# Performance work log

Measured on AMD Instinct MI355X. Metric: run time of the kernel, lower is better.

Reference implementation:

```python
import jax, jax.numpy as jnp
import numpy as np
from jax import lax

STD_H, STD_W = 364, 280
RADIUS, SIGMA = 15, 4.0


def gaussian_kernel():
    r = jnp.arange(-RADIUS, RADIUS + 1, dtype=jnp.float32)
    d2 = r[:, None] ** 2 + r[None, :] ** 2
    k = jnp.exp(-0.5 / (SIGMA ** 2) * d2)
    k = k / k.sum()
    return k[None, None]  # (1,1,31,31) OIHW


def setup_inputs() -> dict:
    key = jax.random.key(0)
    k1, k2 = jax.random.split(key)
    B, H, W = 32, 512, 512
    input_face = jax.random.uniform(k1, (B, 3, H, W), dtype=jnp.float32)
    # landmarks in (x, y) pixel coords within the HxW image
    landmarks = jax.random.uniform(k2, (B, 68, 2), dtype=jnp.float32) * jnp.array([W, H], jnp.float32)
    weight = gaussian_kernel()
    return {"input_face": input_face, "landmarks": landmarks, "weight": weight}


def _blur(x, weight):
    # x: (B,1,h,w), 31x31 'same' conv (kernel symmetric, so corr == conv)
    return lax.conv_general_dilated(x, weight, (1, 1), 'SAME',
                                    dimension_numbers=('NCHW', 'OIHW', 'NCHW'))


def reference(input_face, landmarks, weight):
    B, C, H, W = input_face.shape
    scaling = STD_H / H
    lm = landmarks * scaling                      # (B,68,2) in standard coords
    center = lm[:, 30:31, :]                      # (B,1,2)

    p0 = lm[:, 30:36, :]
    p1 = lm[:, 2:15, :]
    p2 = lm[:, 48:68, :]
    p3 = lm[:, 6:11, :]
    p01 = (p0 - center) * 1.5 + center
    p11 = (p1 - center) * 0.5 + center
    p12 = (p1 - center) * 0.7 + center
    p13 = (p1 - center) * 0.9 + center
    p21 = (p2 - center) * 1.3 + center
    keys = jnp.concatenate([p0, p01, p12, p13, p11, p2, p3, p21], axis=-2)  # (B,96,2)

    iy = jnp.round(jnp.clip(keys[..., 1], 0, STD_H - 1)).astype(jnp.int32)
    ix = jnp.round(jnp.clip(keys[..., 0], 0, STD_W - 1)).astype(jnp.int32)

    # Faithful to torch advanced-indexing semantics: union of ALL batches'
    # points is written into every batch's heatmap.
    hm = jnp.zeros((STD_H, STD_W), jnp.float32).at[iy.ravel(), ix.ravel()].set(1.0)
    hm = jnp.broadcast_to(hm[None, None], (B, 1, STD_H, STD_W))

    w1 = _blur(hm, weight)
    w2 = jnp.where(w1 > 1e-7, 1.0, w1)
    w3 = _blur(w2, weight)

    w_mask = jax.image.resize(w3, (B, 1, H, W), method='bilinear')
    return (1.0 - w_mask) * input_face  # filling='black'
```

## Files before the change

### kernel.cpp

```cpp
#include <hip/hip_runtime.h>

#define BB   32
#define HH   512
#define WW   512
#define SH   364
#define SW   280
#define RAD  15
#define NK   96
#define OMN  (HH*WW)
#define PF4  (OMN/4)

#define OH   16
#define OW   32
#define NRM  13
#define NCM  19
#define WRM  (NRM + 2*RAD)
#define HRM  (NRM + 4*RAD)
#define HCP  84
#define WCP  52
#define NCP  20
#define G1   13
#define G2   5

typedef float f4 __attribute__((ext_vector_type(4)));

__device__ __forceinline__ void point_ij(const float* __restrict__ lm, int b, int j,
                                         int& ix, int& iy) {
    int idx; float s;
    if      (j <  6) { idx = 30 + j;        s = 1.0f; }
    else if (j < 12) { idx = 30 + (j - 6);  s = 1.5f; }
    else if (j < 25) { idx =  2 + (j - 12); s = 0.7f; }
    else if (j < 38) { idx =  2 + (j - 25); s = 0.9f; }
    else if (j < 51) { idx =  2 + (j - 38); s = 0.5f; }
    else if (j < 71) { idx = 48 + (j - 51); s = 1.0f; }
    else if (j < 76) { idx =  6 + (j - 71); s = 1.0f; }
    else             { idx = 48 + (j - 76); s = 1.3f; }
    const float scal = 364.0f / 512.0f;
    float lx = lm[b * 136 + idx * 2 + 0] * scal;
    float ly = lm[b * 136 + idx * 2 + 1] * scal;
    float kx, ky;
    if (s == 1.0f) { kx = lx; ky = ly; }
    else {
        float cx = lm[b * 136 + 30 * 2 + 0] * scal;
        float cy = lm[b * 136 + 30 * 2 + 1] * scal;
        kx = (lx - cx) * s + cx;
        ky = (ly - cy) * s + cy;
    }
    ix = __float2int_rn(fminf(fmaxf(kx, 0.0f), (float)(SW - 1)));
    iy = __float2int_rn(fminf(fmaxf(ky, 0.0f), (float)(SH - 1)));
}

__global__ __launch_bounds__(256, 2) void k_fused(const float* __restrict__ lm,
                                                  const float* __restrict__ wt,
                                                  const f4* __restrict__ face,
                                                  f4* __restrict__ out) {
    __shared__ float gwl[31];
    __shared__ alignas(16) float hmS[HRM][HCP];
    __shared__ alignas(16) float t1 [HRM][WCP];
    __shared__ alignas(16) float w2S[WRM][WCP];
    __shared__ alignas(16) float t2 [WRM][NCP];
    __shared__ alignas(16) float w3S[NRM][NCP];
    __shared__ alignas(16) float maskS[OH][OW];

    const int tid = threadIdx.x;
    const int h0 = blockIdx.y * OH, w0 = blockIdx.x * OW;
    const float sy = (float)SH / (float)HH;
    const float sx = (float)SW / (float)WW;

    const int j   = tid & 127;
    const int grp = tid >> 7;
    const int dh  = j >> 3, dw4 = (j & 7) << 2;
    const long off = (long)(h0 + dh) * (WW / 4) + ((w0 + dw4) >> 2);

    if (tid < 31) gwl[tid] = wt[15 * 31 + tid] / sqrtf(wt[15 * 31 + 15]);

    const int hl = h0 + OH - 1, wl = w0 + OW - 1;
    float fy0 = fmaxf(((float)h0 + 0.5f) * sy - 0.5f, 0.0f);
    float fyl = fminf(((float)hl + 0.5f) * sy - 0.5f, (float)(SH - 1));
    int rbase = (int)fy0;
    int rend  = min(SH - 1, (int)fyl + 1);
    float fx0 = fmaxf(((float)w0 + 0.5f) * sx - 0.5f, 0.0f);
    float fxl = fminf(((float)wl + 0.5f) * sx - 0.5f, (float)(SW - 1));
    int cbase = (int)fx0;
    int cend  = min(SW - 1, (int)fxl + 1);
    int NR = rend - rbase + 1;
    int NC = cend - cbase + 1;
    int HR = NR + 4 * RAD, HC = NC + 4 * RAD;

    for (int i = tid; i < HRM * HCP; i += 256) ((float*)hmS)[i] = 0.0f;
    __syncthreads();

    float g[31];
    #pragma unroll
    for (int k = 0; k < 31; ++k) g[k] = gwl[k];

    for (int p = tid; p < BB * NK; p += 256) {
        int b = p / NK, jj = p - b * NK;
        int ix, iy;
        point_ij(lm, b, jj, ix, iy);
        int ly = iy - (rbase - 2 * RAD), lx = ix - (cbase - 2 * RAD);
        if (ly >= 0 && ly < HR && lx >= 0 && lx < HC) hmS[ly][lx] = 1.0f;
    }

    f4 pf0  = face[(long)(grp +  0) * PF4 + off];
    f4 pf1  = face[(long)(grp +  2) * PF4 + off];
    f4 pf2  = face[(long)(grp +  4) * PF4 + off];
    f4 pf3  = face[(long)(grp +  6) * PF4 + off];
    f4 pf4  = face[(long)(grp +  8) * PF4 + off];
    f4 pf5  = face[(long)(grp + 10) * PF4 + off];
    f4 pf6  = face[(long)(grp + 12) * PF4 + off];
    f4 pf7  = face[(long)(grp + 14) * PF4 + off];
    f4 pf8  = face[(long)(grp + 16) * PF4 + off];
    f4 pf9  = face[(long)(grp + 18) * PF4 + off];
    f4 pf10 = face[(long)(grp + 20) * PF4 + off];
    f4 pf11 = face[(long)(grp + 22) * PF4 + off];
    f4 pf12 = face[(long)(grp + 24) * PF4 + off];
    f4 pf13 = face[(long)(grp + 26) * PF4 + off];
    f4 pf14 = face[(long)(grp + 28) * PF4 + off];
    f4 pf15 = face[(long)(grp + 30) * PF4 + off];

    __syncthreads();

    for (int it = tid; it < HRM * G1; it += 256) {
        int y = it / G1, c0g = it - y * G1;
        f4 rb[9];
        #pragma unroll
        for (int k = 0; k < 9; ++k) rb[k] = *(const f4*)&hmS[y][(c0g + k) * 4];
        float r[36];
        #pragma unroll
        for (int k = 0; k < 9; ++k) {
            r[4*k+0] = rb[k][0]; r[4*k+1] = rb[k][1];
            r[4*k+2] = rb[k][2]; r[4*k+3] = rb[k][3];
        }
        f4 o;
        #pragma unroll
        for (int q = 0; q < 4; ++q) {
            float acc = 0.0f;
            #pragma unroll
            for (int d = 0; d < 31; ++d) acc += g[d] * r[q + d];
            o[q] = acc;
        }
        *(f4*)&t1[y][c0g * 4] = o;
    }
    __syncthreads();

    for (int it = tid; it < WRM * G1; it += 256) {
        int y = it / G1, c0 = (it - y * G1) * 4;
        f4 acc = {0.0f, 0.0f, 0.0f, 0.0f};
        #pragma unroll
        for (int d = 0; d < 31; ++d) {
            f4 v = *(const f4*)&t1[y + d][c0];
            acc += v * g[d];
        }
        int gy = rbase - RAD + y;
        bool rowok = (gy >= 0 && gy < SH);
        f4 o;
        #pragma unroll
        for (int q = 0; q < 4; ++q) {
            float v = acc[q];
            v = (v > 1e-7f) ? 1.0f : v;
            int gx = cbase - RAD + c0 + q;
            o[q] = (rowok && gx >= 0 && gx < SW) ? v : 0.0f;
        }
        *(f4*)&w2S[y][c0] = o;
    }
    __syncthreads();

    for (int it = tid; it < WRM * G2; it += 256) {
        int y = it / G2, c0g = it - y * G2;
        f4 rb[9];
        #pragma unroll
        for (int k = 0; k < 9; ++k) rb[k] = *(const f4*)&w2S[y][(c0g + k) * 4];
        float r[36];
        #pragma unroll
        for (int k = 0; k < 9; ++k) {
            r[4*k+0] = rb[k][0]; r[4*k+1] = rb[k][1];
            r[4*k+2] = rb[k][2]; r[4*k+3] = rb[k][3];
        }
        f4 o;
        #pragma unroll
        for (int q = 0; q < 4; ++q) {
            float acc = 0.0f;
            #pragma unroll
            for (int d = 0; d < 31; ++d) acc += g[d] * r[q + d];
            o[q] = acc;
        }
        *(f4*)&t2[y][c0g * 4] = o;
    }
    __syncthreads();

    for (int it = tid; it < NRM * G2; it += 256) {
        int y = it / G2, c0 = (it - y * G2) * 4;
        f4 acc = {0.0f, 0.0f, 0.0f, 0.0f};
        #pragma unroll
        for (int d = 0; d < 31; ++d) {
            f4 v = *(const f4*)&t2[y + d][c0];
            acc += v * g[d];
        }
        *(f4*)&w3S[y][c0] = acc;
    }
    __syncthreads();

    for (int i = tid; i < OH * OW; i += 256) {
        int ddh = i / OW, ddw = i - ddh * OW;
        int h = h0 + ddh, w = w0 + ddw;
        float fy = fminf(fmaxf(((float)h + 0.5f) * sy - 0.5f, 0.0f), (float)(SH - 1));
        float fx = fminf(fmaxf(((float)w + 0.5f) * sx - 0.5f, 0.0f), (float)(SW - 1));
        int y0 = (int)fy, x0 = (int)fx;
        int y1 = min(y0 + 1, SH - 1), x1 = min(x0 + 1, SW - 1);
        float ty = fy - (float)y0, tx = fx - (float)x0;
        int ly0 = y0 - rbase, ly1 = y1 - rbase;
        int lx0 = x0 - cbase, lx1 = x1 - cbase;
        float v00 = w3S[ly0][lx0], v01 = w3S[ly0][lx1];
        float v10 = w3S[ly1][lx0], v11 = w3S[ly1][lx1];
        float v = (1.0f - ty) * ((1.0f - tx) * v00 + tx * v01)
                +         ty  * ((1.0f - tx) * v10 + tx * v11);
        maskS[ddh][ddw] = 1.0f - v;
    }
    __syncthreads();

    const f4 m = *(const f4*)&maskS[dh][dw4];
    __builtin_nontemporal_store(pf0  * m, &out[(long)(grp +  0) * PF4 + off]);
    __builtin_nontemporal_store(pf1  * m, &out[(long)(grp +  2) * PF4 + off]);
    __builtin_nontemporal_store(pf2  * m, &out[(long)(grp +  4) * PF4 + off]);
    __builtin_nontemporal_store(pf3  * m, &out[(long)(grp +  6) * PF4 + off]);
    __builtin_nontemporal_store(pf4  * m, &out[(long)(grp +  8) * PF4 + off]);
    __builtin_nontemporal_store(pf5  * m, &out[(long)(grp + 10) * PF4 + off]);
    __builtin_nontemporal_store(pf6  * m, &out[(long)(grp + 12) * PF4 + off]);
    __builtin_nontemporal_store(pf7  * m, &out[(long)(grp + 14) * PF4 + off]);
    __builtin_nontemporal_store(pf8  * m, &out[(long)(grp + 16) * PF4 + off]);
    __builtin_nontemporal_store(pf9  * m, &out[(long)(grp + 18) * PF4 + off]);
    __builtin_nontemporal_store(pf10 * m, &out[(long)(grp + 20) * PF4 + off]);
    __builtin_nontemporal_store(pf11 * m, &out[(long)(grp + 22) * PF4 + off]);
    __builtin_nontemporal_store(pf12 * m, &out[(long)(grp + 24) * PF4 + off]);
    __builtin_nontemporal_store(pf13 * m, &out[(long)(grp + 26) * PF4 + off]);
    __builtin_nontemporal_store(pf14 * m, &out[(long)(grp + 28) * PF4 + off]);
    __builtin_nontemporal_store(pf15 * m, &out[(long)(grp + 30) * PF4 + off]);
    #pragma unroll 8
    for (int k = 16; k < 48; ++k) {
        long idx = (long)(grp + 2 * k) * PF4 + off;
        f4 a = face[idx];
        __builtin_nontemporal_store(a * m, &out[idx]);
    }
}

extern "C" void kernel_launch(void* const* d_in, const int* in_sizes, int n_in,
                              void* d_out, int out_size, void* d_ws, size_t ws_size,
                              hipStream_t stream) {
    const float* face = (const float*)d_in[0];
    const float* lm   = (const float*)d_in[1];
    const float* wt   = (const float*)d_in[2];

    k_fused<<<dim3(WW / OW, HH / OH), 256, 0, stream>>>(
        lm, wt, (const f4*)face, (f4*)d_out);
}
```

Before: 50.98 us.

## Double output tile height and alias w2 buffer onto heatmap shared memory

Each block now covers a 32x32 output tile instead of 16x32, so the 31-tap blur halo is amortised over twice as many output pixels and the grid shrinks by half. Each thread now owns one float4 position and loops over all 96 batch-channel planes, instead of splitting planes between two thread groups. To keep shared memory within budget at the larger tile, the w2 buffer reuses the heatmap buffer's storage. The cost is fewer blocks for latency hiding and more serial memory work per thread, and the aliasing is only safe if the heatmap is fully consumed before w2 is written.

```diff
diff --git a/kernel.cpp b/kernel.cpp
--- a/kernel.cpp
+++ b/kernel.cpp
@@ -10,9 +10,9 @@
 #define OMN  (HH*WW)
 #define PF4  (OMN/4)
 
-#define OH   16
+#define OH   32
 #define OW   32
-#define NRM  13
+#define NRM  25
 #define NCM  19
 #define WRM  (NRM + 2*RAD)
 #define HRM  (NRM + 4*RAD)
@@ -57,19 +57,17 @@
     __shared__ float gwl[31];
     __shared__ alignas(16) float hmS[HRM][HCP];
     __shared__ alignas(16) float t1 [HRM][WCP];
-    __shared__ alignas(16) float w2S[WRM][WCP];
     __shared__ alignas(16) float t2 [WRM][NCP];
     __shared__ alignas(16) float w3S[NRM][NCP];
     __shared__ alignas(16) float maskS[OH][OW];
+    float (*w2S)[WCP] = (float(*)[WCP])hmS;
 
     const int tid = threadIdx.x;
     const int h0 = blockIdx.y * OH, w0 = blockIdx.x * OW;
     const float sy = (float)SH / (float)HH;
     const float sx = (float)SW / (float)WW;
 
-    const int j   = tid & 127;
-    const int grp = tid >> 7;
-    const int dh  = j >> 3, dw4 = (j & 7) << 2;
+    const int dh  = tid >> 3, dw4 = (tid & 7) << 2;
     const long off = (long)(h0 + dh) * (WW / 4) + ((w0 + dw4) >> 2);
 
     if (tid < 31) gwl[tid] = wt[15 * 31 + tid] / sqrtf(wt[15 * 31 + 15]);
@@ -102,22 +100,22 @@
         if (ly >= 0 && ly < HR && lx >= 0 && lx < HC) hmS[ly][lx] = 1.0f;
     }
 
-    f4 pf0  = face[(long)(grp +  0) * PF4 + off];
-    f4 pf1  = face[(long)(grp +  2) * PF4 + off];
-    f4 pf2  = face[(long)(grp +  4) * PF4 + off];
-    f4 pf3  = face[(long)(grp +  6) * PF4 + off];
-    f4 pf4  = face[(long)(grp +  8) * PF4 + off];
-    f4 pf5  = face[(long)(grp + 10) * PF4 + off];
-    f4 pf6  = face[(long)(grp + 12) * PF4 + off];
-    f4 pf7  = face[(long)(grp + 14) * PF4 + off];
-    f4 pf8  = face[(long)(grp + 16) * PF4 + off];
-    f4 pf9  = face[(long)(grp + 18) * PF4 + off];
-    f4 pf10 = face[(long)(grp + 20) * PF4 + off];
-    f4 pf11 = face[(long)(grp + 22) * PF4 + off];
-    f4 pf12 = face[(long)(grp + 24) * PF4 + off];
-    f4 pf13 = face[(long)(grp + 26) * PF4 + off];
-    f4 pf14 = face[(long)(grp + 28) * PF4 + off];
-    f4 pf15 = face[(long)(grp + 30) * PF4 + off];
+    f4 pf0  = face[ 0L * PF4 + off];
+    f4 pf1  = face[ 1L * PF4 + off];
+    f4 pf2  = face[ 2L * PF4 + off];
+    f4 pf3  = face[ 3L * PF4 + off];
+    f4 pf4  = face[ 4L * PF4 + off];
+    f4 pf5  = face[ 5L * PF4 + off];
+    f4 pf6  = face[ 6L * PF4 + off];
+    f4 pf7  = face[ 7L * PF4 + off];
+    f4 pf8  = face[ 8L * PF4 + off];
+    f4 pf9  = face[ 9L * PF4 + off];
+    f4 pf10 = face[10L * PF4 + off];
+    f4 pf11 = face[11L * PF4 + off];
+    f4 pf12 = face[12L * PF4 + off];
+    f4 pf13 = face[13L * PF4 + off];
+    f4 pf14 = face[14L * PF4 + off];
+    f4 pf15 = face[15L * PF4 + off];
 
     __syncthreads();
 
@@ -220,25 +218,25 @@
     __syncthreads();
 
     const f4 m = *(const f4*)&maskS[dh][dw4];
-    __builtin_nontemporal_store(pf0  * m, &out[(long)(grp +  0) * PF4 + off]);
-    __builtin_nontemporal_store(pf1  * m, &out[(long)(grp +  2) * PF4 + off]);
-    __builtin_nontemporal_store(pf2  * m, &out[(long)(grp +  4) * PF4 + off]);
-    __builtin_nontemporal_store(pf3  * m, &out[(long)(grp +  6) * PF4 + off]);
-    __builtin_nontemporal_store(pf4  * m, &out[(long)(grp +  8) * PF4 + off]);
-    __builtin_nontemporal_store(pf5  * m, &out[(long)(grp + 10) * PF4 + off]);
-    __builtin_nontemporal_store(pf6  * m, &out[(long)(grp + 12) * PF4 + off]);
-    __builtin_nontemporal_store(pf7  * m, &out[(long)(grp + 14) * PF4 + off]);
-    __builtin_nontemporal_store(pf8  * m, &out[(long)(grp + 16) * PF4 + off]);
-    __builtin_nontemporal_store(pf9  * m, &out[(long)(grp + 18) * PF4 + off]);
-    __builtin_nontemporal_store(pf10 * m, &out[(long)(grp + 20) * PF4 + off]);
-    __builtin_nontemporal_store(pf11 * m, &out[(long)(grp + 22) * PF4 + off]);
-    __builtin_nontemporal_store(pf12 * m, &out[(long)(grp + 24) * PF4 + off]);
-    __builtin_nontemporal_store(pf13 * m, &out[(long)(grp + 26) * PF4 + off]);
-    __builtin_nontemporal_store(pf14 * m, &out[(long)(grp + 28) * PF4 + off]);
-    __builtin_nontemporal_store(pf15 * m, &out[(long)(grp + 30) * PF4 + off]);
+    __builtin_nontemporal_store(pf0  * m, &out[ 0L * PF4 + off]);
+    __builtin_nontemporal_store(pf1  * m, &out[ 1L * PF4 + off]);
+    __builtin_nontemporal_store(pf2  * m, &out[ 2L * PF4 + off]);
+    __builtin_nontemporal_store(pf3  * m, &out[ 3L * PF4 + off]);
+    __builtin_nontemporal_store(pf4  * m, &out[ 4L * PF4 + off]);
+    __builtin_nontemporal_store(pf5  * m, &out[ 5L * PF4 + off]);
+    __builtin_nontemporal_store(pf6  * m, &out[ 6L * PF4 + off]);
+    __builtin_nontemporal_store(pf7  * m, &out[ 7L * PF4 + off]);
+    __builtin_nontemporal_store(pf8  * m, &out[ 8L * PF4 + off]);
+    __builtin_nontemporal_store(pf9  * m, &out[ 9L * PF4 + off]);
+    __builtin_nontemporal_store(pf10 * m, &out[10L * PF4 + off]);
+    __builtin_nontemporal_store(pf11 * m, &out[11L * PF4 + off]);
+    __builtin_nontemporal_store(pf12 * m, &out[12L * PF4 + off]);
+    __builtin_nontemporal_store(pf13 * m, &out[13L * PF4 + off]);
+    __builtin_nontemporal_store(pf14 * m, &out[14L * PF4 + off]);
+    __builtin_nontemporal_store(pf15 * m, &out[15L * PF4 + off]);
     #pragma unroll 8
-    for (int k = 16; k < 48; ++k) {
-        long idx = (long)(grp + 2 * k) * PF4 + off;
+    for (int k = 16; k < 96; ++k) {
+        long idx = (long)k * PF4 + off;
         f4 a = face[idx];
         __builtin_nontemporal_store(a * m, &out[idx]);
     }
```

Measured after the change: 54.71 us. 1.07x slower.
